# Kernel tuning notes

Hardware: AMD Instinct MI355X
Metric: run time of the kernel (lower is better)

Reference implementation:

```python
import jax, jax.numpy as jnp
import numpy as np

B, S, H = 2, 2048, 2048
NH, NKV, HD = 16, 4, 128
THETA = 1000000.0

def _rope_tables(seq_len, dim, theta):
    inv_freq = 1.0 / (theta ** (np.arange(0, dim, 2, dtype=np.float32) / dim))
    t = np.arange(seq_len, dtype=np.float32)
    freqs = np.outer(t, inv_freq)                      # [S, dim/2]
    emb = np.concatenate([freqs, freqs], axis=-1)      # [S, dim]
    return jnp.asarray(np.cos(emb)), jnp.asarray(np.sin(emb))

def setup_inputs() -> dict:
    key = jax.random.key(0)
    ks = jax.random.split(key, 5)
    cos, sin = _rope_tables(S, HD, THETA)
    scale = 1.0 / np.sqrt(H)
    return {
        "x": jax.random.normal(ks[0], (B, S, H), jnp.float32),
        "cos": cos, "sin": sin,
        "wq": jax.random.normal(ks[1], (H, NH * HD), jnp.float32) * scale,
        "wk": jax.random.normal(ks[2], (H, NKV * HD), jnp.float32) * scale,
        "wv": jax.random.normal(ks[3], (H, NKV * HD), jnp.float32) * scale,
        "wo": jax.random.normal(ks[4], (NH * HD, H), jnp.float32) * scale,
    }

def _rotate_half(t):
    h = t.shape[-1] // 2
    return jnp.concatenate([-t[..., h:], t[..., :h]], axis=-1)

def reference(x, cos, sin, wq, wk, wv, wo):
    b, s, _ = x.shape
    n_rep = NH // NKV
    q = (x @ wq).reshape(b, s, NH, HD)    # [b,s,nh,hd]
    k = (x @ wk).reshape(b, s, NKV, HD)
    v = (x @ wv).reshape(b, s, NKV, HD)
    # RoPE: cos/sin [s,hd] broadcast over batch and heads
    c = cos[None, :, None, :]
    sn = sin[None, :, None, :]
    q = q * c + _rotate_half(q) * sn
    k = k * c + _rotate_half(k) * sn
    # GQA: repeat kv heads n_rep times
    k = jnp.repeat(k, n_rep, axis=2)      # [b,s,nh,hd]
    v = jnp.repeat(v, n_rep, axis=2)
    q = q.transpose(0, 2, 1, 3)           # [b,nh,s,hd]
    k = k.transpose(0, 2, 1, 3)
    v = v.transpose(0, 2, 1, 3)
    scores = jnp.einsum('bhqd,bhkd->bhqk', q, k) / jnp.sqrt(jnp.float32(HD))
    causal = jnp.tril(jnp.ones((s, s), dtype=bool))
    scores = jnp.where(causal[None, None], scores, jnp.float32(-jnp.inf))
    attn = jax.nn.softmax(scores.astype(jnp.float32), axis=-1).astype(q.dtype)
    out = jnp.einsum('bhqk,bhkd->bhqd', attn, v)
    out = out.transpose(0, 2, 1, 3).reshape(b, s, NH * HD)
    return out @ wo
```

## Files before the change

kernel.cpp:

```cpp
#include <hip/hip_runtime.h>
#include <hip/hip_bf16.h>

#define Bb 2
#define Ss 2048
#define Hh 2048
#define NH 16
#define NKV 4
#define HD 128
#define NREP (NH / NKV)
#define Mrows (Bb * Ss)
#define NQKV (NH*HD + 2*NKV*HD)

using short8 = __attribute__((ext_vector_type(8))) short;
using f32x4  = __attribute__((ext_vector_type(4))) float;

__device__ __forceinline__ unsigned short f2b(float f) {
  union { float f; unsigned u; } v; v.f = f;
  return (unsigned short)((v.u + 0x7fffu + ((v.u >> 16) & 1u)) >> 16);
}

__device__ __forceinline__ void gload16(const void* g, void* l) {
  __builtin_amdgcn_global_load_lds(
      (const __attribute__((address_space(1))) unsigned int*)g,
      (__attribute__((address_space(3))) unsigned int*)l, 16, 0, 0);
}

__global__ void cvt_bf16(const float* __restrict__ in, unsigned short* __restrict__ out, int n) {
  int i = (blockIdx.x * blockDim.x + threadIdx.x) * 4;
  if (i < n) {
    float4 f = *(const float4*)(in + i);
    ushort4 o;
    o.x = f2b(f.x); o.y = f2b(f.y); o.z = f2b(f.z); o.w = f2b(f.w);
    *(ushort4*)(out + i) = o;
  }
}

__global__ void transpose_cvt(const float* __restrict__ in, unsigned short* __restrict__ out,
                              int R, int C) {
  __shared__ float tile[32][33];
  int c0 = blockIdx.x * 32, r0 = blockIdx.y * 32;
  int tx = threadIdx.x, ty = threadIdx.y;
  #pragma unroll
  for (int i = ty; i < 32; i += 8)
    tile[i][tx] = in[(long)(r0 + i) * C + c0 + tx];
  __syncthreads();
  #pragma unroll
  for (int i = ty; i < 32; i += 8)
    out[(long)(c0 + i) * R + r0 + tx] = f2b(tile[tx][i]);
}

__global__ void transpose_qkv(const float* __restrict__ wq, const float* __restrict__ wk,
                              const float* __restrict__ wv, unsigned short* __restrict__ outT) {
  __shared__ float tile[32][33];
  int n0 = blockIdx.x * 32, k0 = blockIdx.y * 32;
  const float* src; int c0, C;
  if (n0 < Hh)            { src = wq; c0 = n0;            C = NH * HD; }
  else if (n0 < Hh + 512) { src = wk; c0 = n0 - Hh;       C = NKV * HD; }
  else                    { src = wv; c0 = n0 - Hh - 512; C = NKV * HD; }
  int tx = threadIdx.x, ty = threadIdx.y;
  #pragma unroll
  for (int i = ty; i < 32; i += 8)
    tile[i][tx] = src[(long)(k0 + i) * C + c0 + tx];
  __syncthreads();
  #pragma unroll
  for (int i = ty; i < 32; i += 8)
    outT[(long)(n0 + i) * Hh + k0 + tx] = f2b(tile[tx][i]);
}

__global__ __launch_bounds__(256) void gemm_qkv(const unsigned short* __restrict__ A,
                                                const unsigned short* __restrict__ Bt,
                                                const float* __restrict__ cosT,
                                                const float* __restrict__ sinT,
                                                unsigned short* __restrict__ qt,
                                                unsigned short* __restrict__ kt,
                                                unsigned short* __restrict__ vt) {
  __shared__ unsigned short As[128 * 64];
  __shared__ unsigned short Bs[128 * 64];
  const int t = threadIdx.x;
  const int lane = t & 63, wave = t >> 6;
  const int quad = lane >> 4, l16 = lane & 15;
  const int tile = blockIdx.x >> 5;
  const int n0 = tile * 128, m0 = (blockIdx.x & 31) * 128;
  const int wm = wave * 32;
  const bool isv = tile >= 20;
  const int Kk = Hh;

  f32x4 acc[2][8] = {};

  const int srow = t >> 3;
  const int sgr  = (t & 7) ^ (srow & 7);
  const unsigned short* Ag = A  + (long)(m0 + srow) * Kk + sgr * 8;
  const unsigned short* Bg = Bt + (long)(n0 + srow) * Kk + sgr * 8;
  unsigned short* lA = As + (wave * 64) * 8;
  unsigned short* lB = Bs + (wave * 64) * 8;

  for (int k0 = 0; k0 < Kk; k0 += 64) {
    #pragma unroll
    for (int i = 0; i < 4; i++)
      gload16(Ag + (long)i * 32 * Kk + k0, lA + i * 256 * 8);
    #pragma unroll
    for (int i = 0; i < 4; i++)
      gload16(Bg + (long)i * 32 * Kk + k0, lB + i * 256 * 8);
    __syncthreads();

    #pragma unroll
    for (int sub = 0; sub < 2; sub++) {
      short8 af[2], bf[8];
      #pragma unroll
      for (int i = 0; i < 2; i++)
        af[i] = *(const short8*)(As + (wm + i * 16 + l16) * 64 + (((sub * 4 + quad) ^ (l16 & 7)) * 8));
      #pragma unroll
      for (int i = 0; i < 8; i++)
        bf[i] = *(const short8*)(Bs + (i * 16 + l16) * 64 + (((sub * 4 + quad) ^ (l16 & 7)) * 8));

      if (isv) {
        #pragma unroll
        for (int mi = 0; mi < 2; mi++)
          #pragma unroll
          for (int ni = 0; ni < 8; ni++)
            acc[mi][ni] = __builtin_amdgcn_mfma_f32_16x16x32_bf16(bf[ni], af[mi], acc[mi][ni], 0, 0, 0);
      } else {
        #pragma unroll
        for (int mi = 0; mi < 2; mi++)
          #pragma unroll
          for (int ni = 0; ni < 8; ni++)
            acc[mi][ni] = __builtin_amdgcn_mfma_f32_16x16x32_bf16(af[mi], bf[ni], acc[mi][ni], 0, 0, 0);
      }
    }
    __syncthreads();
  }

  if (!isv) {
    const bool isq = tile < 16;
    const int hh = isq ? tile : tile - 16;
    #pragma unroll
    for (int mi = 0; mi < 2; mi++)
      #pragma unroll
      for (int r = 0; r < 4; r++) {
        int srw = m0 + wm + mi * 16 + quad * 4 + r;
        int bb = srw >> 11, s = srw & (Ss - 1);
        unsigned short* dst = isq ? qt + (((long)bb * NH + hh) * Ss + s) * HD
                                  : kt + (((long)bb * NKV + hh) * Ss + s) * HD;
        const float* cr = cosT + (long)s * HD;
        const float* sr = sinT + (long)s * HD;
        #pragma unroll
        for (int ni = 0; ni < 4; ni++) {
          int d = ni * 16 + l16;
          float cc = cr[d], sn = sr[d];
          float x0 = acc[mi][ni][r], x1 = acc[mi][ni + 4][r];
          dst[d]      = f2b(x0 * cc - x1 * sn);
          dst[d + 64] = f2b(x1 * cc + x0 * sn);
        }
      }
  } else {
    const int kvh = tile - 20;
    const int bb = m0 >> 11;
    #pragma unroll
    for (int mi = 0; mi < 2; mi++)
      #pragma unroll
      for (int ni = 0; ni < 8; ni++)
        #pragma unroll
        for (int r = 0; r < 4; r++) {
          int d = ni * 16 + quad * 4 + r;
          int s = (m0 + wm + mi * 16 + l16) & (Ss - 1);
          vt[(((long)bb * NKV + kvh) * HD + d) * Ss + s] = f2b(acc[mi][ni][r]);
        }
  }
}

__global__ __launch_bounds__(256) void gemm_bt(const unsigned short* __restrict__ A,
                                               const unsigned short* __restrict__ Bt,
                                               float* __restrict__ Cv,
                                               int Mm, int Nn, int Kk) {
  __shared__ unsigned short As[128 * 64];
  __shared__ unsigned short Bs[128 * 64];
  const int t = threadIdx.x;
  const int lane = t & 63, wave = t >> 6;
  const int quad = lane >> 4, l16 = lane & 15;
  const int n0 = (blockIdx.x >> 5) * 128, m0 = (blockIdx.x & 31) * 128;
  const int wm = (wave >> 1) * 64, wn = (wave & 1) * 64;

  f32x4 acc[4][4] = {};

  const int srow = t >> 3;
  const int sgr  = (t & 7) ^ (srow & 7);
  const unsigned short* Ag = A  + (long)(m0 + srow) * Kk + sgr * 8;
  const unsigned short* Bg = Bt + (long)(n0 + srow) * Kk + sgr * 8;
  unsigned short* lA = As + (wave * 64) * 8;
  unsigned short* lB = Bs + (wave * 64) * 8;

  for (int k0 = 0; k0 < Kk; k0 += 64) {
    #pragma unroll
    for (int i = 0; i < 4; i++)
      gload16(Ag + (long)i * 32 * Kk + k0, lA + i * 256 * 8);
    #pragma unroll
    for (int i = 0; i < 4; i++)
      gload16(Bg + (long)i * 32 * Kk + k0, lB + i * 256 * 8);
    __syncthreads();

    #pragma unroll
    for (int sub = 0; sub < 2; sub++) {
      short8 af[4], bf[4];
      #pragma unroll
      for (int i = 0; i < 4; i++)
        af[i] = *(const short8*)(As + (wm + i * 16 + l16) * 64 + (((sub * 4 + quad) ^ (l16 & 7)) * 8));
      #pragma unroll
      for (int i = 0; i < 4; i++)
        bf[i] = *(const short8*)(Bs + (wn + i * 16 + l16) * 64 + (((sub * 4 + quad) ^ (l16 & 7)) * 8));

      #pragma unroll
      for (int mi = 0; mi < 4; mi++)
        #pragma unroll
        for (int ni = 0; ni < 4; ni++)
          acc[mi][ni] = __builtin_amdgcn_mfma_f32_16x16x32_bf16(af[mi], bf[ni], acc[mi][ni], 0, 0, 0);
    }
    __syncthreads();
  }

  #pragma unroll
  for (int mi = 0; mi < 4; mi++)
    #pragma unroll
    for (int ni = 0; ni < 4; ni++)
      #pragma unroll
      for (int r = 0; r < 4; r++) {
        long row = m0 + wm + mi * 16 + quad * 4 + r;
        long col = n0 + wn + ni * 16 + l16;
        Cv[row * Nn + col] = acc[mi][ni][r];
      }
}

__global__ __launch_bounds__(256, 2) void flash_attn(const unsigned short* __restrict__ qt,
                                                     const unsigned short* __restrict__ kt,
                                                     const unsigned short* __restrict__ vt,
                                                     unsigned short* __restrict__ out) {
  __shared__ unsigned short Ks[2][64 * 128];
  __shared__ unsigned short Vs[2][128 * 64];

  const int w = threadIdx.x >> 6, lane = threadIdx.x & 63;
  const int quad = lane >> 4, l16 = lane & 15;
  const int r8 = lane >> 3, c8 = lane & 7;
  const int idx = blockIdx.x;
  const int t5 = idx >> 5;
  const int qblk = (idx < 256) ? (15 - t5) : (t5 - 8);
  const int bh = idx & 31;
  const int h = bh & (NH - 1), b = bh >> 4;
  const int q0w = qblk * 128 + w * 32;
  const int kvh = h / NREP;

  const unsigned short* Qb = qt + ((long)b * NH + h) * Ss * HD;
  const unsigned short* Kb = kt + ((long)b * NKV + kvh) * Ss * HD;
  const unsigned short* Vb = vt + ((long)b * NKV + kvh) * HD * Ss;
  const int nch = (qblk + 1) * 2;

  #pragma unroll
  for (int i = 0; i < 4; i++) {
    int rho = i * 16 + w * 4 + quad;
    int key = (rho & 32) + ((rho >> 2) & 3) * 8 + ((rho >> 4) & 1) * 4 + (rho & 3);
    int sg = l16 ^ (w * 4 + quad);
    gload16(Kb + (long)key * HD + sg * 8, &Ks[0][(i * 256 + w * 64) * 8]);
  }
  #pragma unroll
  for (int i = 0; i < 4; i++) {
    int dv = i * 32 + w * 8 + r8;
    int sg = c8 ^ r8;
    gload16(Vb + (long)dv * Ss + sg * 8, &Vs[0][(i * 256 + w * 64) * 8]);
  }

  short8 qf[2][4];
  #pragma unroll
  for (int qi = 0; qi < 2; qi++)
    #pragma unroll
    for (int kc = 0; kc < 4; kc++)
      qf[qi][kc] = *(const short8*)(Qb + (long)(q0w + qi * 16 + l16) * HD + kc * 32 + quad * 8);

  f32x4 accO[2][8] = {};
  float m_i[2], l_i[2];
  m_i[0] = m_i[1] = -__builtin_inff();
  l_i[0] = l_i[1] = 0.f;
  const float cscale = 1.4426950408889634f * 0.08838834764831845f;

  for (int c = 0; c < nch; ++c) {
    const unsigned short* Ksb = Ks[c & 1];
    const unsigned short* Vsb = Vs[c & 1];

    if (c + 1 < nch) {
      const int k0 = (c + 1) * 64;
      unsigned short* Kd = Ks[(c + 1) & 1];
      unsigned short* Vd = Vs[(c + 1) & 1];
      #pragma unroll
      for (int i = 0; i < 4; i++) {
        int rho = i * 16 + w * 4 + quad;
        int key = (rho & 32) + ((rho >> 2) & 3) * 8 + ((rho >> 4) & 1) * 4 + (rho & 3);
        int sg = l16 ^ (w * 4 + quad);
        gload16(Kb + (long)(k0 + key) * HD + sg * 8, Kd + (i * 256 + w * 64) * 8);
      }
      #pragma unroll
      for (int i = 0; i < 4; i++) {
        int dv = i * 32 + w * 8 + r8;
        int sg = c8 ^ r8;
        gload16(Vb + (long)dv * Ss + k0 + sg * 8, Vd + (i * 256 + w * 64) * 8);
      }
      asm volatile("s_waitcnt vmcnt(8)" ::: "memory");
    } else {
      asm volatile("s_waitcnt vmcnt(0)" ::: "memory");
    }
    asm volatile("s_barrier" ::: "memory");

    if (c * 64 < q0w + 32) {
      f32x4 sc[2][4] = {};
      #pragma unroll
      for (int T = 0; T < 4; T++)
        #pragma unroll
        for (int kc = 0; kc < 4; kc++) {
          short8 kf = *(const short8*)(Ksb + ((16 * T + l16) * 16 + ((kc * 4 + quad) ^ l16)) * 8);
          #pragma unroll
          for (int qi = 0; qi < 2; qi++)
            sc[qi][T] = __builtin_amdgcn_mfma_f32_16x16x32_bf16(kf, qf[qi][kc], sc[qi][T], 0, 0, 0);
        }

      if ((c + 1) * 64 - 1 > q0w) {
        #pragma unroll
        for (int qi = 0; qi < 2; qi++) {
          int qq = q0w + qi * 16 + l16;
          #pragma unroll
          for (int T = 0; T < 4; T++)
            #pragma unroll
            for (int r = 0; r < 4; r++) {
              int ka = c * 64 + (T >> 1) * 32 + quad * 8 + (T & 1) * 4 + r;
              if (ka > qq) sc[qi][T][r] = -__builtin_inff();
            }
        }
      }

      short8 pf[2][2];
      #pragma unroll
      for (int qi = 0; qi < 2; qi++) {
        float v = sc[qi][0][0];
        #pragma unroll
        for (int T = 0; T < 4; T++)
          #pragma unroll
          for (int r = 0; r < 4; r++) v = fmaxf(v, sc[qi][T][r]);
        v = fmaxf(v, __shfl_xor(v, 16));
        v = fmaxf(v, __shfl_xor(v, 32));
        float mn = fmaxf(m_i[qi], v);
        float alpha = __builtin_amdgcn_exp2f((m_i[qi] - mn) * cscale);
        m_i[qi] = mn;
        l_i[qi] *= alpha;
        #pragma unroll
        for (int Dt = 0; Dt < 8; Dt++)
          #pragma unroll
          for (int r = 0; r < 4; r++) accO[qi][Dt][r] *= alpha;

        float p[4][4], rs = 0.f;
        #pragma unroll
        for (int T = 0; T < 4; T++)
          #pragma unroll
          for (int r = 0; r < 4; r++) {
            p[T][r] = __builtin_amdgcn_exp2f((sc[qi][T][r] - mn) * cscale);
            rs += p[T][r];
          }
        rs += __shfl_xor(rs, 16);
        rs += __shfl_xor(rs, 32);
        l_i[qi] += rs;

        #pragma unroll
        for (int c2 = 0; c2 < 2; c2++) {
          short8 f;
          f[0] = (short)f2b(p[2 * c2][0]);     f[1] = (short)f2b(p[2 * c2][1]);
          f[2] = (short)f2b(p[2 * c2][2]);     f[3] = (short)f2b(p[2 * c2][3]);
          f[4] = (short)f2b(p[2 * c2 + 1][0]); f[5] = (short)f2b(p[2 * c2 + 1][1]);
          f[6] = (short)f2b(p[2 * c2 + 1][2]); f[7] = (short)f2b(p[2 * c2 + 1][3]);
          pf[qi][c2] = f;
        }
      }

      #pragma unroll
      for (int c2 = 0; c2 < 2; c2++)
        #pragma unroll
        for (int Dt = 0; Dt < 8; Dt++) {
          short8 vf = *(const short8*)(Vsb + ((16 * Dt + l16) * 8 + ((4 * c2 + quad) ^ (l16 & 7))) * 8);
          #pragma unroll
          for (int qi = 0; qi < 2; qi++)
            accO[qi][Dt] = __builtin_amdgcn_mfma_f32_16x16x32_bf16(vf, pf[qi][c2], accO[qi][Dt], 0, 0, 0);
        }
    }

    asm volatile("s_waitcnt lgkmcnt(0)" ::: "memory");
    asm volatile("s_barrier" ::: "memory");
  }

  #pragma unroll
  for (int qi = 0; qi < 2; qi++) {
    float inv = 1.f / l_i[qi];
    long orow = (long)b * Ss + q0w + qi * 16 + l16;
    #pragma unroll
    for (int Dt = 0; Dt < 8; Dt++) {
      ushort4 o;
      o.x = f2b(accO[qi][Dt][0] * inv);
      o.y = f2b(accO[qi][Dt][1] * inv);
      o.z = f2b(accO[qi][Dt][2] * inv);
      o.w = f2b(accO[qi][Dt][3] * inv);
      *(ushort4*)(out + orow * (NH * HD) + h * HD + Dt * 16 + quad * 4) = o;
    }
  }
}

extern "C" void kernel_launch(void* const* d_in, const int* in_sizes, int n_in,
                              void* d_out, int out_size, void* d_ws, size_t ws_size,
                              hipStream_t stream) {
  const float* x    = (const float*)d_in[0];
  const float* cosT = (const float*)d_in[1];
  const float* sinT = (const float*)d_in[2];
  const float* wq   = (const float*)d_in[3];
  const float* wk   = (const float*)d_in[4];
  const float* wv   = (const float*)d_in[5];
  const float* wo   = (const float*)d_in[6];
  float* out = (float*)d_out;

  char* ws = (char*)d_ws;
  unsigned short* xb    = (unsigned short*)(ws);
  unsigned short* wqkvt = (unsigned short*)(ws + (16l << 20));
  unsigned short* wot   = (unsigned short*)(ws + (28l << 20));
  unsigned short* qt    = (unsigned short*)(ws + (36l << 20));
  unsigned short* kt    = (unsigned short*)(ws + (52l << 20));
  unsigned short* vt    = (unsigned short*)(ws + (56l << 20));
  unsigned short* attno = xb;

  cvt_bf16<<<Mrows * Hh / 4 / 256, 256, 0, stream>>>(x, xb, Mrows * Hh);

  dim3 tb(32, 8);
  transpose_qkv<<<dim3(NQKV / 32, Hh / 32), tb, 0, stream>>>(wq, wk, wv, wqkvt);
  transpose_cvt<<<dim3(Hh / 32, Hh / 32), tb, 0, stream>>>(wo, wot, Hh, Hh);

  gemm_qkv<<<(NQKV / 128) * (Mrows / 128), 256, 0, stream>>>(xb, wqkvt, cosT, sinT, qt, kt, vt);

  flash_attn<<<(Ss / 128) * NH * Bb, 256, 0, stream>>>(qt, kt, vt, attno);

  gemm_bt<<<(Hh / 128) * (Mrows / 128), 256, 0, stream>>>(attno, wot, out, Mrows, Hh, Hh);
}
```

Before: 321.0 us.

## Single-buffer V in flash attention for higher occupancy and remap blocks per XCD

Flash attention now keeps a single V buffer in shared memory. V for the current chunk is loaded at the start of each iteration, and an extra barrier before the PV matmul overlaps that load with the QK^T and softmax work. The smaller LDS footprint lets launch bounds rise to 3 blocks per CU. Blocks in flash attention and both GEMMs are also remapped so that blocks on the same XCD share a KV head or weight tile, aiming for better L2 reuse. The cost is an extra barrier per chunk and exposed V latency if the softmax phase is too short to hide it.

```diff
diff --git a/kernel.cpp b/kernel.cpp
--- a/kernel.cpp
+++ b/kernel.cpp
@@ -79,8 +79,9 @@
   const int t = threadIdx.x;
   const int lane = t & 63, wave = t >> 6;
   const int quad = lane >> 4, l16 = lane & 15;
-  const int tile = blockIdx.x >> 5;
-  const int n0 = tile * 128, m0 = (blockIdx.x & 31) * 128;
+  const int xcd = blockIdx.x & 7, slot = blockIdx.x >> 3;
+  const int tile = xcd * 3 + (slot >> 5);
+  const int n0 = tile * 128, m0 = (slot & 31) * 128;
   const int wm = wave * 32;
   const bool isv = tile >= 20;
   const int Kk = Hh;
@@ -177,7 +178,8 @@
   const int t = threadIdx.x;
   const int lane = t & 63, wave = t >> 6;
   const int quad = lane >> 4, l16 = lane & 15;
-  const int n0 = (blockIdx.x >> 5) * 128, m0 = (blockIdx.x & 31) * 128;
+  const int xcd = blockIdx.x & 7, slot = blockIdx.x >> 3;
+  const int n0 = (xcd * 2 + (slot >> 5)) * 128, m0 = (slot & 31) * 128;
   const int wm = (wave >> 1) * 64, wn = (wave & 1) * 64;
 
   f32x4 acc[4][4] = {};
@@ -229,41 +231,40 @@
       }
 }
 
-__global__ __launch_bounds__(256, 2) void flash_attn(const unsigned short* __restrict__ qt,
+__global__ __launch_bounds__(256, 3) void flash_attn(const unsigned short* __restrict__ qt,
                                                      const unsigned short* __restrict__ kt,
                                                      const unsigned short* __restrict__ vt,
                                                      unsigned short* __restrict__ out) {
   __shared__ unsigned short Ks[2][64 * 128];
-  __shared__ unsigned short Vs[2][128 * 64];
+  __shared__ unsigned short Vs[128 * 64];
 
   const int w = threadIdx.x >> 6, lane = threadIdx.x & 63;
   const int quad = lane >> 4, l16 = lane & 15;
   const int r8 = lane >> 3, c8 = lane & 7;
   const int idx = blockIdx.x;
-  const int t5 = idx >> 5;
-  const int qblk = (idx < 256) ? (15 - t5) : (t5 - 8);
-  const int bh = idx & 31;
-  const int h = bh & (NH - 1), b = bh >> 4;
+  const int xcd = idx & 7;
+  const int b = xcd >> 2, kvh = xcd & 3;
+  const int rest = idx >> 3;
+  const int k16 = rest >> 2;
+  const int qblk = (k16 < 8) ? (15 - k16) : (k16 - 8);
+  const int h = kvh * NREP + (rest & 3);
   const int q0w = qblk * 128 + w * 32;
-  const int kvh = h / NREP;
 
   const unsigned short* Qb = qt + ((long)b * NH + h) * Ss * HD;
   const unsigned short* Kb = kt + ((long)b * NKV + kvh) * Ss * HD;
   const unsigned short* Vb = vt + ((long)b * NKV + kvh) * HD * Ss;
   const int nch = (qblk + 1) * 2;
 
+  const int rho = (w * 4 + quad);
+  const int sgK = l16 ^ (w * 4 + quad);
+  const int dvr = w * 8 + r8;
+  const int sgV = c8 ^ r8;
+
   #pragma unroll
   for (int i = 0; i < 4; i++) {
-    int rho = i * 16 + w * 4 + quad;
-    int key = (rho & 32) + ((rho >> 2) & 3) * 8 + ((rho >> 4) & 1) * 4 + (rho & 3);
-    int sg = l16 ^ (w * 4 + quad);
-    gload16(Kb + (long)key * HD + sg * 8, &Ks[0][(i * 256 + w * 64) * 8]);
-  }
-  #pragma unroll
-  for (int i = 0; i < 4; i++) {
-    int dv = i * 32 + w * 8 + r8;
-    int sg = c8 ^ r8;
-    gload16(Vb + (long)dv * Ss + sg * 8, &Vs[0][(i * 256 + w * 64) * 8]);
+    int rr = i * 16 + rho;
+    int key = (rr & 32) + ((rr >> 2) & 3) * 8 + ((rr >> 4) & 1) * 4 + (rr & 3);
+    gload16(Kb + (long)key * HD + sgK * 8, &Ks[0][(i * 256 + w * 64) * 8]);
   }
 
   short8 qf[2][4];
@@ -281,32 +282,33 @@
 
   for (int c = 0; c < nch; ++c) {
     const unsigned short* Ksb = Ks[c & 1];
-    const unsigned short* Vsb = Vs[c & 1];
-
+
+    {
+      const int k0v = c * 64;
+      #pragma unroll
+      for (int i = 0; i < 4; i++) {
+        int dv = i * 32 + dvr;
+        gload16(Vb + (long)dv * Ss + k0v + sgV * 8, Vs + (i * 256 + w * 64) * 8);
+      }
+    }
     if (c + 1 < nch) {
       const int k0 = (c + 1) * 64;
       unsigned short* Kd = Ks[(c + 1) & 1];
-      unsigned short* Vd = Vs[(c + 1) & 1];
       #pragma unroll
       for (int i = 0; i < 4; i++) {
-        int rho = i * 16 + w * 4 + quad;
-        int key = (rho & 32) + ((rho >> 2) & 3) * 8 + ((rho >> 4) & 1) * 4 + (rho & 3);
-        int sg = l16 ^ (w * 4 + quad);
-        gload16(Kb + (long)(k0 + key) * HD + sg * 8, Kd + (i * 256 + w * 64) * 8);
-      }
-      #pragma unroll
-      for (int i = 0; i < 4; i++) {
-        int dv = i * 32 + w * 8 + r8;
-        int sg = c8 ^ r8;
-        gload16(Vb + (long)dv * Ss + k0 + sg * 8, Vd + (i * 256 + w * 64) * 8);
+        int rr = i * 16 + rho;
+        int key = (rr & 32) + ((rr >> 2) & 3) * 8 + ((rr >> 4) & 1) * 4 + (rr & 3);
+        gload16(Kb + (long)(k0 + key) * HD + sgK * 8, Kd + (i * 256 + w * 64) * 8);
       }
       asm volatile("s_waitcnt vmcnt(8)" ::: "memory");
     } else {
-      asm volatile("s_waitcnt vmcnt(0)" ::: "memory");
+      asm volatile("s_waitcnt vmcnt(4)" ::: "memory");
     }
     asm volatile("s_barrier" ::: "memory");
 
-    if (c * 64 < q0w + 32) {
+    const bool active = (c * 64 < q0w + 32);
+    short8 pf[2][2];
+    if (active) {
       f32x4 sc[2][4] = {};
       #pragma unroll
       for (int T = 0; T < 4; T++)
@@ -332,7 +334,6 @@
         }
       }
 
-      short8 pf[2][2];
       #pragma unroll
       for (int qi = 0; qi < 2; qi++) {
         float v = sc[qi][0][0];
@@ -373,12 +374,20 @@
           pf[qi][c2] = f;
         }
       }
-
+    }
+
+    if (c + 1 < nch)
+      asm volatile("s_waitcnt vmcnt(4)" ::: "memory");
+    else
+      asm volatile("s_waitcnt vmcnt(0)" ::: "memory");
+    asm volatile("s_barrier" ::: "memory");
+
+    if (active) {
       #pragma unroll
       for (int c2 = 0; c2 < 2; c2++)
         #pragma unroll
         for (int Dt = 0; Dt < 8; Dt++) {
-          short8 vf = *(const short8*)(Vsb + ((16 * Dt + l16) * 8 + ((4 * c2 + quad) ^ (l16 & 7))) * 8);
+          short8 vf = *(const short8*)(Vs + ((16 * Dt + l16) * 8 + ((4 * c2 + quad) ^ (l16 & 7))) * 8);
           #pragma unroll
           for (int qi = 0; qi < 2; qi++)
             accO[qi][Dt] = __builtin_amdgcn_mfma_f32_16x16x32_bf16(vf, pf[qi][c2], accO[qi][Dt], 0, 0, 0);
```

Result: slower. 397.5 us (+23.8%).

## Fuse prep kernels into one launch and group attention blocks by KV head per XCD

Applied to the files above, without the earlier changes.

Merges the x conversion and the two weight transpose-convert kernels into a single prep kernel that dispatches on block index, removing two kernel launches and their tail gaps. It also remaps flash-attention block indices so each XCD (idx & 7) handles one (batch, KV-head) pair. The four query heads sharing a KV head then run on the same XCD and can reuse K/V from its L2. The causal heavy-first ordering is kept through k16. The risk is that the new mapping changes the load balance across XCDs.

```diff
diff --git a/kernel.cpp b/kernel.cpp
--- a/kernel.cpp
+++ b/kernel.cpp
@@ -25,46 +25,47 @@
       (__attribute__((address_space(3))) unsigned int*)l, 16, 0, 0);
 }
 
-__global__ void cvt_bf16(const float* __restrict__ in, unsigned short* __restrict__ out, int n) {
-  int i = (blockIdx.x * blockDim.x + threadIdx.x) * 4;
-  if (i < n) {
-    float4 f = *(const float4*)(in + i);
+__global__ void prep(const float* __restrict__ x, unsigned short* __restrict__ xb,
+                     const float* __restrict__ wq, const float* __restrict__ wk,
+                     const float* __restrict__ wv, unsigned short* __restrict__ wqkvt,
+                     const float* __restrict__ wo, unsigned short* __restrict__ wot) {
+  __shared__ float tile[32][33];
+  const int bid = blockIdx.x;
+  const int t = threadIdx.x;
+  if (bid < 8192) {
+    int i = (bid * 256 + t) * 4;
+    float4 f = *(const float4*)(x + i);
     ushort4 o;
     o.x = f2b(f.x); o.y = f2b(f.y); o.z = f2b(f.z); o.w = f2b(f.w);
-    *(ushort4*)(out + i) = o;
-  }
-}
-
-__global__ void transpose_cvt(const float* __restrict__ in, unsigned short* __restrict__ out,
-                              int R, int C) {
-  __shared__ float tile[32][33];
-  int c0 = blockIdx.x * 32, r0 = blockIdx.y * 32;
-  int tx = threadIdx.x, ty = threadIdx.y;
-  #pragma unroll
-  for (int i = ty; i < 32; i += 8)
-    tile[i][tx] = in[(long)(r0 + i) * C + c0 + tx];
-  __syncthreads();
-  #pragma unroll
-  for (int i = ty; i < 32; i += 8)
-    out[(long)(c0 + i) * R + r0 + tx] = f2b(tile[tx][i]);
-}
-
-__global__ void transpose_qkv(const float* __restrict__ wq, const float* __restrict__ wk,
-                              const float* __restrict__ wv, unsigned short* __restrict__ outT) {
-  __shared__ float tile[32][33];
-  int n0 = blockIdx.x * 32, k0 = blockIdx.y * 32;
-  const float* src; int c0, C;
-  if (n0 < Hh)            { src = wq; c0 = n0;            C = NH * HD; }
-  else if (n0 < Hh + 512) { src = wk; c0 = n0 - Hh;       C = NKV * HD; }
-  else                    { src = wv; c0 = n0 - Hh - 512; C = NKV * HD; }
-  int tx = threadIdx.x, ty = threadIdx.y;
-  #pragma unroll
-  for (int i = ty; i < 32; i += 8)
-    tile[i][tx] = src[(long)(k0 + i) * C + c0 + tx];
-  __syncthreads();
-  #pragma unroll
-  for (int i = ty; i < 32; i += 8)
-    outT[(long)(n0 + i) * Hh + k0 + tx] = f2b(tile[tx][i]);
+    *(ushort4*)(xb + i) = o;
+    return;
+  }
+  const int tx = t & 31, ty = t >> 5;
+  if (bid < 8192 + 6144) {
+    int idx = bid - 8192;
+    int n0 = (idx % 96) * 32, k0 = (idx / 96) * 32;
+    const float* src; int c0, C;
+    if (n0 < Hh)            { src = wq; c0 = n0;            C = NH * HD; }
+    else if (n0 < Hh + 512) { src = wk; c0 = n0 - Hh;       C = NKV * HD; }
+    else                    { src = wv; c0 = n0 - Hh - 512; C = NKV * HD; }
+    #pragma unroll
+    for (int i = ty; i < 32; i += 8)
+      tile[i][tx] = src[(long)(k0 + i) * C + c0 + tx];
+    __syncthreads();
+    #pragma unroll
+    for (int i = ty; i < 32; i += 8)
+      wqkvt[(long)(n0 + i) * Hh + k0 + tx] = f2b(tile[tx][i]);
+  } else {
+    int idx = bid - 8192 - 6144;
+    int n0 = (idx % 64) * 32, k0 = (idx / 64) * 32;
+    #pragma unroll
+    for (int i = ty; i < 32; i += 8)
+      tile[i][tx] = wo[(long)(k0 + i) * Hh + n0 + tx];
+    __syncthreads();
+    #pragma unroll
+    for (int i = ty; i < 32; i += 8)
+      wot[(long)(n0 + i) * Hh + k0 + tx] = f2b(tile[tx][i]);
+  }
 }
 
 __global__ __launch_bounds__(256) void gemm_qkv(const unsigned short* __restrict__ A,
@@ -240,12 +241,13 @@
   const int quad = lane >> 4, l16 = lane & 15;
   const int r8 = lane >> 3, c8 = lane & 7;
   const int idx = blockIdx.x;
-  const int t5 = idx >> 5;
-  const int qblk = (idx < 256) ? (15 - t5) : (t5 - 8);
-  const int bh = idx & 31;
-  const int h = bh & (NH - 1), b = bh >> 4;
+  const int xcd = idx & 7;
+  const int b = xcd >> 2, kvh = xcd & 3;
+  const int rest = idx >> 3;
+  const int k16 = rest >> 2;
+  const int qblk = (k16 < 8) ? (15 - k16) : (k16 - 8);
+  const int h = kvh * NREP + (rest & 3);
   const int q0w = qblk * 128 + w * 32;
-  const int kvh = h / NREP;
 
   const unsigned short* Qb = qt + ((long)b * NH + h) * Ss * HD;
   const unsigned short* Kb = kt + ((long)b * NKV + kvh) * Ss * HD;
@@ -426,11 +428,7 @@
   unsigned short* vt    = (unsigned short*)(ws + (56l << 20));
   unsigned short* attno = xb;
 
-  cvt_bf16<<<Mrows * Hh / 4 / 256, 256, 0, stream>>>(x, xb, Mrows * Hh);
-
-  dim3 tb(32, 8);
-  transpose_qkv<<<dim3(NQKV / 32, Hh / 32), tb, 0, stream>>>(wq, wk, wv, wqkvt);
-  transpose_cvt<<<dim3(Hh / 32, Hh / 32), tb, 0, stream>>>(wo, wot, Hh, Hh);
+  prep<<<8192 + 6144 + 4096, 256, 0, stream>>>(x, xb, wq, wk, wv, wqkvt, wo, wot);
 
   gemm_qkv<<<(NQKV / 128) * (Mrows / 128), 256, 0, stream>>>(xb, wqkvt, cosT, sinT, qt, kt, vt);
 
```

Result: no change. 317.5 us (-1.1%).
